# Performance work log

Hardware: AMD Instinct MI355X
Metric: run time of the kernel (lower is better)

## Reference

```python
import jax, jax.numpy as jnp
import numpy as np
from jax import lax

NB, D_MODEL, D_INNER, D_STATE, K, L, BATCH, NCLS, DT_RANK = 3, 512, 1024, 8, 4, 2048, 4, 10, 32


def setup_inputs() -> dict:
    key = jax.random.key(0)
    ks = jax.random.split(key, 12)
    s = 0.02
    inp = {
        "x": jax.random.normal(ks[0], (BATCH, L, D_MODEL), jnp.float32),
        "in_proj_w": s * jax.random.normal(ks[1], (NB, D_MODEL, 2 * D_INNER), jnp.float32),
        "conv_w": s * jax.random.normal(ks[2], (NB, D_INNER, K), jnp.float32),
        "conv_b": jnp.zeros((NB, D_INNER), jnp.float32),
        "x_proj_w": s * jax.random.normal(ks[3], (NB, D_INNER, DT_RANK + 2 * D_STATE), jnp.float32),
        "dt_proj_w": s * jax.random.normal(ks[4], (NB, DT_RANK, D_INNER), jnp.float32),
        "dt_proj_b": jnp.full((NB, D_INNER), -4.0, jnp.float32),
        "A_log": jnp.broadcast_to(jnp.log(jnp.arange(1, D_STATE + 1, dtype=jnp.float32)), (NB, D_INNER, D_STATE)).copy(),
        "D": jnp.ones((NB, D_INNER), jnp.float32),
        "out_proj_w": s * jax.random.normal(ks[5], (NB, D_INNER, D_MODEL), jnp.float32),
        "cls_w": s * jax.random.normal(ks[6], (D_MODEL, NCLS), jnp.float32),
        "cls_b": jnp.zeros((NCLS,), jnp.float32),
    }
    return inp


def _mamba_block(x, Wi, cw, cb, Wx, Wdt, bdt, A_log, Dp, Wo):
    # x: [B, L, d_model]
    Bsz, Lx, _ = x.shape
    d_inner = Dp.shape[0]
    d_state = A_log.shape[-1]
    dt_rank = Wdt.shape[0]
    xz = x @ Wi                               # [B, L, 2*d_inner]
    u, z = jnp.split(xz, 2, axis=-1)
    # causal depthwise conv1d over time
    uc = jnp.swapaxes(u, 1, 2)                # [B, d_inner, L]
    k = cw.shape[-1]
    uc = lax.conv_general_dilated(uc, cw[:, None, :], window_strides=(1,),
                                  padding=[(k - 1, 0)], feature_group_count=d_inner,
                                  dimension_numbers=("NCH", "OIH", "NCH"))
    u = jax.nn.silu(jnp.swapaxes(uc, 1, 2) + cb)   # [B, L, d_inner]
    dbl = u @ Wx                                   # [B, L, dt_rank + 2*d_state]
    dt = dbl[..., :dt_rank]
    Bm = dbl[..., dt_rank:dt_rank + d_state]
    Cm = dbl[..., dt_rank + d_state:]
    delta = jax.nn.softplus(dt @ Wdt + bdt)        # [B, L, d_inner]
    A = -jnp.exp(A_log)                            # [d_inner, d_state]

    def step(h, inp):
        d_t, B_t, C_t, u_t = inp                   # [B,d],[B,n],[B,n],[B,d]
        h = jnp.exp(d_t[..., None] * A) * h + (d_t * u_t)[..., None] * B_t[:, None, :]
        return h, jnp.einsum("bdn,bn->bd", h, C_t)

    xs = (jnp.swapaxes(delta, 0, 1), jnp.swapaxes(Bm, 0, 1),
          jnp.swapaxes(Cm, 0, 1), jnp.swapaxes(u, 0, 1))
    h0 = jnp.zeros((Bsz, d_inner, d_state), x.dtype)
    _, ys = lax.scan(step, h0, xs)                 # ys: [L, B, d_inner]
    y = jnp.swapaxes(ys, 0, 1) + u * Dp
    y = y * jax.nn.silu(z)
    return x + y @ Wo                              # residual


def reference(x, in_proj_w, conv_w, conv_b, x_proj_w, dt_proj_w, dt_proj_b, A_log, D, out_proj_w, cls_w, cls_b):
    nb = in_proj_w.shape[0]
    for i in range(nb):
        x = _mamba_block(x, in_proj_w[i], conv_w[i], conv_b[i], x_proj_w[i],
                         dt_proj_w[i], dt_proj_b[i], A_log[i], D[i], out_proj_w[i])
    pooled = jnp.mean(x, axis=1)                   # AdaptiveAvgPool1d(1) over seq
    return pooled @ cls_w + cls_b                  # [B, num_classes]
```

## Files before the change

### kernel.cpp

```cpp
#include <hip/hip_runtime.h>
#include <cstddef>
#include <cstdint>

#define L_SEQ   2048
#define BATCH_N 4
#define DMODEL  512
#define DINNER  1024
#define DSTATE  8
#define KCONV   4
#define DTRANK  32
#define NBLK    3
#define NCLS_N  10
#define MROWS   (BATCH_N * L_SEQ)
#define DBLW    48
#define NSPLIT  8

#define LC2 16
#define NC2 (L_SEQ / LC2)
#define DHALF (DINNER / 2)
#define SCAN_THREADS 512
#define SCAN_WAVES   (SCAN_THREADS / 64)

#define CGRP 8
#define CPG  (NC2 / CGRP)

typedef __attribute__((ext_vector_type(8))) short bf16x8;
typedef __attribute__((ext_vector_type(4))) short bf16x4;
typedef __attribute__((ext_vector_type(2))) short bf16x2;
typedef __attribute__((ext_vector_type(4))) float f32x4;

__device__ __forceinline__ float sigmoid_fast(float x) { return 1.f / (1.f + __expf(-x)); }
__device__ __forceinline__ float silu_fast(float x)    { return x * sigmoid_fast(x); }
__device__ __forceinline__ float softplus_fast(float x){
    return fmaxf(x, 0.f) + __logf(1.f + __expf(-fabsf(x)));
}
__device__ __forceinline__ float exp2_fast(float x) {
#if __has_builtin(__builtin_amdgcn_exp2f)
    return __builtin_amdgcn_exp2f(x);
#else
    return __expf(x * 0.69314718055994531f);
#endif
}
#define LOG2E 1.44269504088896341f

__device__ __forceinline__ unsigned short f2bf(float f) {
    union { float f; uint32_t u; } v; v.f = f;
    const uint32_t u = v.u;
    return (unsigned short)((u + 0x7fffu + ((u >> 16) & 1u)) >> 16);
}
__device__ __forceinline__ float bf2f(unsigned short h) {
    union { uint32_t u; float f; } v; v.u = ((uint32_t)h) << 16;
    return v.f;
}
__device__ __forceinline__ float bf2f_s(short h) { return bf2f((unsigned short)h); }

__device__ __forceinline__ void load_lds16(const void* g, void* l) {
    __builtin_amdgcn_global_load_lds(
        (const __attribute__((address_space(1))) unsigned int*)g,
        (__attribute__((address_space(3))) unsigned int*)l,
        16, 0, 0);
}

template <int K, int NT, int EPI>
__global__ __launch_bounds__(256) void gemm_bf16(
    const unsigned short* __restrict__ A, int lda,
    const unsigned short* __restrict__ Bt, int ldb,
    int ldc,
    unsigned short* __restrict__ Obf,
    float* __restrict__ pool)
{
    constexpr int BCH   = NT / 8;
    constexpr int NTW   = NT / 32;
    constexpr int STAGE = 8192 + NT * 64;
    constexpr int EPIL  = 128 * (NT + 8);
    constexpr int SMEM  = (STAGE > EPIL) ? STAGE : EPIL;
    __shared__ unsigned short sMem[SMEM];
    unsigned short* sA = sMem;
    unsigned short* sB = sMem + 8192;

    const int tid  = threadIdx.x;
    const int lane = tid & 63;
    const int wave = tid >> 6;

    const int nwgx = gridDim.x;
    const int nwg  = nwgx * gridDim.y;
    int flat = blockIdx.y * nwgx + blockIdx.x;
    {
        const int q = nwg >> 3, r = nwg & 7;
        const int xcd = flat & 7, lid = flat >> 3;
        flat = (xcd < r ? xcd * (q + 1) : r * (q + 1) + (xcd - r) * q) + lid;
    }
    const int m0 = (flat / nwgx) * 128;
    const int n0 = (flat % nwgx) * NT;

    const int wm = (wave >> 1) * 64;
    const int wn = (wave & 1) * (NT / 2);
    const int lm = lane & 15;
    const int lq = lane >> 4;

    const int srow = lane >> 3;
    const int scol = ((lane & 7) ^ srow) * 8;

    f32x4 acc[4][NTW];
    #pragma unroll
    for (int i = 0; i < 4; ++i)
        #pragma unroll
        for (int j = 0; j < NTW; ++j) acc[i][j] = (f32x4){0.f, 0.f, 0.f, 0.f};

    for (int k0 = 0; k0 < K; k0 += 64) {
        #pragma unroll
        for (int c = wave; c < 16; c += 4)
            load_lds16(A + (size_t)(m0 + c * 8 + srow) * lda + k0 + scol, &sA[c * 512]);
        #pragma unroll
        for (int c = wave; c < BCH; c += 4)
            load_lds16(Bt + (size_t)(n0 + c * 8 + srow) * ldb + k0 + scol, &sB[c * 512]);
        __syncthreads();
        #pragma unroll
        for (int ks = 0; ks < 2; ++ks) {
            bf16x8 aF[4], bF[NTW];
            #pragma unroll
            for (int mt = 0; mt < 4; ++mt) {
                const int row = wm + mt * 16 + lm;
                aF[mt] = *(const bf16x8*)&sA[row * 64 + (((ks * 4 + lq) ^ (lm & 7)) * 8)];
            }
            #pragma unroll
            for (int nt = 0; nt < NTW; ++nt) {
                const int row = wn + nt * 16 + lm;
                bF[nt] = *(const bf16x8*)&sB[row * 64 + (((ks * 4 + lq) ^ (lm & 7)) * 8)];
            }
            #pragma unroll
            for (int mt = 0; mt < 4; ++mt)
                #pragma unroll
                for (int nt = 0; nt < NTW; ++nt)
                    acc[mt][nt] = __builtin_amdgcn_mfma_f32_16x16x32_bf16(
                        aF[mt], bF[nt], acc[mt][nt], 0, 0, 0);
        }
        __syncthreads();
    }

    unsigned short* sOut = sMem;
    #pragma unroll
    for (int mt = 0; mt < 4; ++mt) {
        #pragma unroll
        for (int nt = 0; nt < NTW; ++nt) {
            #pragma unroll
            for (int r = 0; r < 4; ++r) {
                const int row = wm + mt * 16 + lq * 4 + r;
                const int col = wn + nt * 16 + lm;
                float v = acc[mt][nt][r];
                if (EPI >= 2) {
                    const size_t gi = (size_t)(m0 + row) * ldc + n0 + col;
                    v += bf2f(Obf[gi]);
                }
                sOut[row * (NT + 8) + col] = f2bf(v);
            }
        }
    }
    __syncthreads();
    #pragma unroll
    for (int j = 0; j < NT / 16; ++j) {
        const int idx = j * 256 + tid;
        const int row = idx / (NT / 8);
        const int cpos = (idx % (NT / 8)) * 8;
        *(bf16x8*)&Obf[(size_t)(m0 + row) * ldc + n0 + cpos] =
            *(const bf16x8*)&sOut[row * (NT + 8) + cpos];
    }
    if (EPI == 3) {
        const int b = m0 >> 11;
        const int col = tid & (NT - 1);
        const int q = tid / NT;
        constexpr int RPQ = 128 / (256 / NT);
        float s = 0.f;
        #pragma unroll
        for (int r = q * RPQ; r < (q + 1) * RPQ; ++r)
            s += bf2f(sOut[r * (NT + 8) + col]);
        atomicAdd(&pool[b * DMODEL + n0 + col], s);
    }
}

__global__ __launch_bounds__(256) void conv_xproj_kernel(
    const unsigned short* __restrict__ xz,
    const float* __restrict__ cwt,
    const float* __restrict__ cb,
    const unsigned short* __restrict__ Wxt,
    unsigned short* __restrict__ ub,
    float* __restrict__ Xp)
{
    __shared__ unsigned short sU[64 * 128];
    const int tid = threadIdx.x, lane = tid & 63, wave = tid >> 6;
    const int lm = lane & 15, lq = lane >> 4;
    const int row0 = blockIdx.x * 64;
    const int split = blockIdx.y;
    const int k0 = split * (DINNER / NSPLIT);

    const int cj  = tid & 15;
    const int rr0 = tid >> 4;
    const int dcol = k0 + cj * 8;
    float4 cb0 = *(const float4*)&cb[dcol];
    float4 cb1 = *(const float4*)&cb[dcol + 4];
    float4 w0[KCONV], w1[KCONV];
    #pragma unroll
    for (int k = 0; k < KCONV; ++k) {
        w0[k] = *(const float4*)&cwt[k * DINNER + dcol];
        w1[k] = *(const float4*)&cwt[k * DINNER + dcol + 4];
    }
    #pragma unroll
    for (int p = 0; p < 4; ++p) {
        const int rl = p * 16 + rr0;
        const int m  = row0 + rl;
        const int t  = m & (L_SEQ - 1);
        float acc[8];
        acc[0] = cb0.x; acc[1] = cb0.y; acc[2] = cb0.z; acc[3] = cb0.w;
        acc[4] = cb1.x; acc[5] = cb1.y; acc[6] = cb1.z; acc[7] = cb1.w;
        #pragma unroll
        for (int k = 0; k < KCONV; ++k) {
            if (t + k - (KCONV - 1) >= 0) {
                bf16x8 xv = *(const bf16x8*)&xz[(size_t)(m + k - (KCONV - 1)) * (2 * DINNER) + dcol];
                acc[0] = fmaf(bf2f_s(xv[0]), w0[k].x, acc[0]);
                acc[1] = fmaf(bf2f_s(xv[1]), w0[k].y, acc[1]);
                acc[2] = fmaf(bf2f_s(xv[2]), w0[k].z, acc[2]);
                acc[3] = fmaf(bf2f_s(xv[3]), w0[k].w, acc[3]);
                acc[4] = fmaf(bf2f_s(xv[4]), w1[k].x, acc[4]);
                acc[5] = fmaf(bf2f_s(xv[5]), w1[k].y, acc[5]);
                acc[6] = fmaf(bf2f_s(xv[6]), w1[k].z, acc[6]);
                acc[7] = fmaf(bf2f_s(xv[7]), w1[k].w, acc[7]);
            }
        }
        bf16x8 o;
        #pragma unroll
        for (int j = 0; j < 8; ++j) o[j] = (short)f2bf(silu_fast(acc[j]));
        *(bf16x8*)&ub[(size_t)m * DINNER + dcol] = o;
        *(bf16x8*)&sU[rl * 128 + ((cj ^ (rl & 7)) * 8)] = o;
    }
    __syncthreads();

    const int rowA = row0 + wave * 16;
    f32x4 acc3[3];
    #pragma unroll
    for (int j = 0; j < 3; ++j) acc3[j] = (f32x4){0.f, 0.f, 0.f, 0.f};

    #pragma unroll
    for (int kk = 0; kk < DINNER / NSPLIT; kk += 32) {
        const int rl = wave * 16 + lm;
        bf16x8 aF = *(const bf16x8*)&sU[rl * 128 + ((((kk >> 3) + lq) ^ (lm & 7)) * 8)];
        bf16x8 bF[3];
        #pragma unroll
        for (int nt = 0; nt < 3; ++nt)
            bF[nt] = *(const bf16x8*)&Wxt[(size_t)(nt * 16 + lm) * DINNER + k0 + kk + lq * 8];
        #pragma unroll
        for (int nt = 0; nt < 3; ++nt)
            acc3[nt] = __builtin_amdgcn_mfma_f32_16x16x32_bf16(
                aF, bF[nt], acc3[nt], 0, 0, 0);
    }
    float* dst = Xp + (size_t)split * MROWS * DBLW;
    #pragma unroll
    for (int nt = 0; nt < 3; ++nt)
        #pragma unroll
        for (int r = 0; r < 4; ++r)
            dst[(size_t)(rowA + lq * 4 + r) * DBLW + nt * 16 + lm] = acc3[nt][r];
}

__global__ __launch_bounds__(256) void xp_reduce(
    const float* __restrict__ Xp, float* __restrict__ dblsum)
{
    const int i = blockIdx.x * 256 + threadIdx.x;
    f32x4 s = (f32x4){0.f, 0.f, 0.f, 0.f};
    #pragma unroll
    for (int sp = 0; sp < NSPLIT; ++sp)
        s += ((const f32x4*)(Xp + (size_t)sp * MROWS * DBLW))[i];
    ((f32x4*)dblsum)[i] = s;
}

__global__ void prep_negA(const float* __restrict__ A_log, float* __restrict__ negA) {
    const int i = blockIdx.x * 256 + threadIdx.x;
    if (i < NBLK * DINNER * DSTATE)
        negA[i] = -__expf(A_log[i]) * LOG2E;
}

__global__ __launch_bounds__(256) void transpose_cast(
    const float* __restrict__ in, unsigned short* __restrict__ out,
    int Kdim, int Ndim, size_t in_stride, size_t out_stride)
{
    __shared__ float s[32][33];
    const float* ip = in + blockIdx.z * in_stride;
    unsigned short* op = out + blockIdx.z * out_stride;
    const int bx = blockIdx.x * 32;
    const int by = blockIdx.y * 32;
    const int t = threadIdx.x;
    const int r = t >> 3;
    const int c4 = (t & 7) * 4;

    const int row = by + r;
    if (bx + c4 + 3 < Ndim) {
        float4 v = *(const float4*)&ip[(size_t)row * Ndim + bx + c4];
        s[r][c4 + 0] = v.x; s[r][c4 + 1] = v.y; s[r][c4 + 2] = v.z; s[r][c4 + 3] = v.w;
    } else {
        for (int i = 0; i < 4; ++i) {
            const int col = bx + c4 + i;
            s[r][c4 + i] = (col < Ndim) ? ip[(size_t)row * Ndim + col] : 0.f;
        }
    }
    __syncthreads();
    if (bx + r < Ndim) {
        unsigned short w0 = f2bf(s[c4 + 0][r]), w1 = f2bf(s[c4 + 1][r]);
        unsigned short w2 = f2bf(s[c4 + 2][r]), w3 = f2bf(s[c4 + 3][r]);
        uint2 pk;
        pk.x = (uint32_t)w0 | ((uint32_t)w1 << 16);
        pk.y = (uint32_t)w2 | ((uint32_t)w3 << 16);
        *(uint2*)&op[(size_t)(bx + r) * Kdim + by + c4] = pk;
    }
}

__global__ void cast_init(const float* __restrict__ in, unsigned short* __restrict__ outb,
                          float* __restrict__ pooled_accum, int n4) {
    const int i = blockIdx.x * 256 + threadIdx.x;
    if (i < BATCH_N * DMODEL / 4)
        ((f32x4*)pooled_accum)[i] = (f32x4){0.f, 0.f, 0.f, 0.f};
    if (i >= n4) return;
    float4 v = ((const float4*)in)[i];
    uint2 pk;
    pk.x = (uint32_t)f2bf(v.x) | ((uint32_t)f2bf(v.y) << 16);
    pk.y = (uint32_t)f2bf(v.z) | ((uint32_t)f2bf(v.w) << 16);
    ((uint2*)outb)[i] = pk;
}

__global__ void conv_w_transpose(const float* __restrict__ cw, float* __restrict__ cwt) {
    const int i = blockIdx.x * 256 + threadIdx.x;
    if (i >= NBLK * DINNER * KCONV) return;
    const int blk = i >> 12;
    const int rem = i & 4095;
    const int d = rem >> 2;
    const int k = rem & 3;
    cwt[blk * 4096 + k * DINNER + d] = cw[blk * 4096 + d * KCONV + k];
}

__device__ __forceinline__ void dt_recompute_lds(
    unsigned short* sDelta,
    const float* __restrict__ dblsum,
    const unsigned short* __restrict__ Wdtt,
    const float* __restrict__ bdt,
    size_t m0, int lane, int wave, int dbase)
{
    const int lm = lane & 15, lq = lane >> 4;
    bf16x8 aF;
    {
        const float* p = &dblsum[(m0 + lm) * DBLW + lq * 8];
        float4 x0 = *(const float4*)p;
        float4 x1 = *(const float4*)(p + 4);
        aF[0] = (short)f2bf(x0.x); aF[1] = (short)f2bf(x0.y);
        aF[2] = (short)f2bf(x0.z); aF[3] = (short)f2bf(x0.w);
        aF[4] = (short)f2bf(x1.x); aF[5] = (short)f2bf(x1.y);
        aF[6] = (short)f2bf(x1.z); aF[7] = (short)f2bf(x1.w);
    }
    constexpr int NPW = DHALF / (16 * SCAN_WAVES);
    #pragma unroll
    for (int nt = 0; nt < NPW; ++nt) {
        const int cloc = wave * (DHALF / SCAN_WAVES) + nt * 16;
        const int col16 = dbase + cloc;
        bf16x8 bF = *(const bf16x8*)&Wdtt[(size_t)(col16 + lm) * DTRANK + lq * 8];
        f32x4 acc = (f32x4){0.f, 0.f, 0.f, 0.f};
        acc = __builtin_amdgcn_mfma_f32_16x16x32_bf16(aF, bF, acc, 0, 0, 0);
        const float bias = bdt[col16 + lm];
        #pragma unroll
        for (int r = 0; r < 4; ++r)
            sDelta[(lq * 4 + r) * DHALF + cloc + lm] =
                f2bf(softplus_fast(acc[r] + bias));
    }
}

__device__ __forceinline__ bool a_is_arange(const float* a) {
    bool pw = true;
    #pragma unroll
    for (int n = 1; n < DSTATE; ++n)
        pw = pw && (fabsf(a[n] - (float)(n + 1) * a[0]) <=
                    1e-5f * (float)(n + 1) * fabsf(a[0]));
    return pw;
}

__global__ __launch_bounds__(SCAN_THREADS) void scan_chunk_kernel(
    const unsigned short* __restrict__ ub,
    const float* __restrict__ dblsum,
    const unsigned short* __restrict__ Wdtt,
    const float* __restrict__ bdt,
    const float* __restrict__ negA,
    float* __restrict__ PSbuf)
{
    const int c  = blockIdx.x;
    const int dh = blockIdx.y;
    const int b  = blockIdx.z;
    const int tid = threadIdx.x;
    const int lane = tid & 63;
    const int wave = tid >> 6;
    const int dbase = dh * DHALF;
    const int d = dbase + tid;

    __shared__ unsigned short sDelta[LC2 * DHALF];
    __shared__ float sB[LC2][DSTATE];

    const size_t m0 = (size_t)b * L_SEQ + c * LC2;

    dt_recompute_lds(sDelta, dblsum, Wdtt, bdt, m0, lane, wave, dbase);
    if (tid < LC2 * DSTATE) {
        const int r = tid >> 3, n = tid & 7;
        sB[r][n] = dblsum[(m0 + r) * DBLW + DTRANK + n];
    }
    __syncthreads();

    float a[DSTATE], S[DSTATE];
    {
        float4 a0 = *(const float4*)&negA[(size_t)d * DSTATE];
        float4 a1 = *(const float4*)&negA[(size_t)d * DSTATE + 4];
        a[0] = a0.x; a[1] = a0.y; a[2] = a0.z; a[3] = a0.w;
        a[4] = a1.x; a[5] = a1.y; a[6] = a1.z; a[7] = a1.w;
    }
    #pragma unroll
    for (int n = 0; n < DSTATE; ++n) S[n] = 0.f;
    float dtsum = 0.f;

    if (a_is_arange(a)) {
        for (int r = 0; r < LC2; ++r) {
            const size_t m = m0 + r;
            const float dt = bf2f(sDelta[r * DHALF + tid]);
            const float du = dt * bf2f(ub[m * DINNER + d]);
            dtsum += dt;
            const float e1 = exp2_fast(dt * a[0]);
            float e = e1;
            #pragma unroll
            for (int n = 0; n < DSTATE; ++n) {
                S[n] = fmaf(e, S[n], du * sB[r][n]);
                e *= e1;
            }
        }
        const size_t nb = (size_t)(b * NC2 + c) * DSTATE;
        const float P1 = exp2_fast(a[0] * dtsum);
        float p = P1;
        #pragma unroll
        for (int n = 0; n < DSTATE; ++n) {
            float2 ps; ps.x = p; ps.y = S[n];
            *(float2*)&PSbuf[(nb + n) * (DINNER * 2) + (size_t)d * 2] = ps;
            p *= P1;
        }
    } else {
        for (int r = 0; r < LC2; ++r) {
            const size_t m = m0 + r;
            const float dt = bf2f(sDelta[r * DHALF + tid]);
            const float du = dt * bf2f(ub[m * DINNER + d]);
            dtsum += dt;
            #pragma unroll
            for (int n = 0; n < DSTATE; ++n) {
                const float e = exp2_fast(dt * a[n]);
                S[n] = fmaf(e, S[n], du * sB[r][n]);
            }
        }
        const size_t nb = (size_t)(b * NC2 + c) * DSTATE;
        #pragma unroll
        for (int n = 0; n < DSTATE; ++n) {
            float2 ps; ps.x = exp2_fast(a[n] * dtsum); ps.y = S[n];
            *(float2*)&PSbuf[(nb + n) * (DINNER * 2) + (size_t)d * 2] = ps;
        }
    }
}

__global__ __launch_bounds__(512) void scan_combine_kernel(
    const float* __restrict__ PSbuf,
    float* __restrict__ Hbuf)
{
    const int dl = threadIdx.x & 63;
    const int g  = threadIdx.x >> 6;
    const int d  = blockIdx.x * 64 + dl;
    const int n  = blockIdx.y;
    const int b  = blockIdx.z;

    __shared__ float sP[CGRP][64];
    __shared__ float sS[CGRP][64];

    const int c0 = g * CPG;
    float Pseg = 1.f, Sseg = 0.f;
    #pragma unroll 4
    for (int cc = 0; cc < CPG; ++cc) {
        const size_t row = (size_t)(b * NC2 + c0 + cc) * DSTATE + n;
        const float2 ps = *(const float2*)&PSbuf[row * (DINNER * 2) + (size_t)d * 2];
        Pseg *= ps.x;
        Sseg = fmaf(ps.x, Sseg, ps.y);
    }
    sP[g][dl] = Pseg;
    sS[g][dl] = Sseg;
    __syncthreads();

    float h = 0.f;
    for (int gg = 0; gg < g; ++gg)
        h = fmaf(sP[gg][dl], h, sS[gg][dl]);

    #pragma unroll 4
    for (int cc = 0; cc < CPG; ++cc) {
        const size_t row = (size_t)(b * NC2 + c0 + cc) * DSTATE + n;
        const float2 ps = *(const float2*)&PSbuf[row * (DINNER * 2) + (size_t)d * 2];
        Hbuf[row * DINNER + d] = h;
        h = fmaf(ps.x, h, ps.y);
    }
}

__global__ __launch_bounds__(SCAN_THREADS) void scan_out_kernel(
    const unsigned short* __restrict__ ub,
    const float* __restrict__ dblsum,
    const unsigned short* __restrict__ Wdtt,
    const float* __restrict__ bdt,
    const unsigned short* __restrict__ xz,
    const float* __restrict__ negA,
    const float* __restrict__ Dp,
    const float* __restrict__ Hin,
    unsigned short* __restrict__ ybuf)
{
    const int c  = blockIdx.x;
    const int dh = blockIdx.y;
    const int b  = blockIdx.z;
    const int tid = threadIdx.x;
    const int lane = tid & 63;
    const int wave = tid >> 6;
    const int dbase = dh * DHALF;
    const int d = dbase + tid;

    __shared__ unsigned short sDelta[LC2 * DHALF];
    __shared__ float sB[LC2][DSTATE];
    __shared__ float sC[LC2][DSTATE];

    const size_t m0 = (size_t)b * L_SEQ + c * LC2;

    dt_recompute_lds(sDelta, dblsum, Wdtt, bdt, m0, lane, wave, dbase);
    if (tid < LC2 * 2 * DSTATE) {
        const int r = tid >> 4, j = tid & 15;
        const float v = dblsum[(m0 + r) * DBLW + DTRANK + j];
        if (j < DSTATE) sB[r][j] = v;
        else            sC[r][j - DSTATE] = v;
    }
    __syncthreads();

    float a[DSTATE], h[DSTATE];
    {
        float4 a0 = *(const float4*)&negA[(size_t)d * DSTATE];
        float4 a1 = *(const float4*)&negA[(size_t)d * DSTATE + 4];
        a[0] = a0.x; a[1] = a0.y; a[2] = a0.z; a[3] = a0.w;
        a[4] = a1.x; a[5] = a1.y; a[6] = a1.z; a[7] = a1.w;
    }
    const size_t base = ((size_t)(b * NC2 + c) * DSTATE) * DINNER + d;
    #pragma unroll
    for (int n = 0; n < DSTATE; ++n)
        h[n] = Hin[base + (size_t)n * DINNER];
    const float Dd = Dp[d];

    if (a_is_arange(a)) {
        for (int r = 0; r < LC2; ++r) {
            const size_t m = m0 + r;
            const float dt = bf2f(sDelta[r * DHALF + tid]);
            const float ut = bf2f(ub[m * DINNER + d]);
            const float zt = bf2f(xz[m * (2 * DINNER) + DINNER + d]);
            const float du = dt * ut;
            const float e1 = exp2_fast(dt * a[0]);
            float e = e1;
            float acc = 0.f;
            #pragma unroll
            for (int n = 0; n < DSTATE; ++n) {
                h[n] = fmaf(e, h[n], du * sB[r][n]);
                acc = fmaf(h[n], sC[r][n], acc);
                e *= e1;
            }
            ybuf[m * DINNER + d] = f2bf(fmaf(ut, Dd, acc) * silu_fast(zt));
        }
    } else {
        for (int r = 0; r < LC2; ++r) {
            const size_t m = m0 + r;
            const float dt = bf2f(sDelta[r * DHALF + tid]);
            const float ut = bf2f(ub[m * DINNER + d]);
            const float zt = bf2f(xz[m * (2 * DINNER) + DINNER + d]);
            const float du = dt * ut;
            float acc = 0.f;
            #pragma unroll
            for (int n = 0; n < DSTATE; ++n) {
                const float e = exp2_fast(dt * a[n]);
                h[n] = fmaf(e, h[n], du * sB[r][n]);
                acc = fmaf(h[n], sC[r][n], acc);
            }
            ybuf[m * DINNER + d] = f2bf(fmaf(ut, Dd, acc) * silu_fast(zt));
        }
    }
}

__global__ __launch_bounds__(512) void pool_cls_kernel(
    const float* __restrict__ pooled_accum,
    const float* __restrict__ w,
    const float* __restrict__ bias,
    float* __restrict__ out)
{
    __shared__ float sp[DMODEL];
    const int b = blockIdx.x;
    const int dm = threadIdx.x;
    sp[dm] = pooled_accum[b * DMODEL + dm] * (1.f / (float)L_SEQ);
    __syncthreads();
    if (dm < NCLS_N) {
        float acc = bias[dm];
        for (int k = 0; k < DMODEL; ++k)
            acc = fmaf(sp[k], w[k * NCLS_N + dm], acc);
        out[b * NCLS_N + dm] = acc;
    }
}

extern "C" void kernel_launch(void* const* d_in, const int* in_sizes, int n_in,
                              void* d_out, int out_size, void* d_ws, size_t ws_size,
                              hipStream_t stream) {
    const float* x_in      = (const float*)d_in[0];
    const float* in_proj_w = (const float*)d_in[1];
    const float* conv_w    = (const float*)d_in[2];
    const float* conv_b    = (const float*)d_in[3];
    const float* x_proj_w  = (const float*)d_in[4];
    const float* dt_proj_w = (const float*)d_in[5];
    const float* dt_proj_b = (const float*)d_in[6];
    const float* A_log     = (const float*)d_in[7];
    const float* Dp        = (const float*)d_in[8];
    const float* out_proj_w= (const float*)d_in[9];
    const float* cls_w     = (const float*)d_in[10];
    const float* cls_b     = (const float*)d_in[11];
    float* out = (float*)d_out;

    char* w = (char*)d_ws;
    auto alloc = [&](size_t bytes) { char* p = w; w += (bytes + 255) & ~(size_t)255; return p; };
    unsigned short* xz_bf  = (unsigned short*)alloc((size_t)MROWS * 2 * DINNER * 2);
    unsigned short* ub     = (unsigned short*)alloc((size_t)MROWS * DINNER * 2);
    float*          Xp     = (float*)         alloc((size_t)NSPLIT * MROWS * DBLW * 4);
    float*          dblsum = (float*)         alloc((size_t)MROWS * DBLW * 4);
    float*          PSbuf  = (float*)         alloc((size_t)BATCH_N * NC2 * DSTATE * DINNER * 2 * 4);
    float*          Hbuf   = (float*)         alloc((size_t)BATCH_N * NC2 * DSTATE * DINNER * 4);
    unsigned short* xb     = (unsigned short*)alloc((size_t)MROWS * DMODEL * 2);
    unsigned short* ybuf   = (unsigned short*)alloc((size_t)MROWS * DINNER * 2);
    unsigned short* Wit    = (unsigned short*)alloc((size_t)NBLK * 2048 * 512 * 2);
    unsigned short* Wot    = (unsigned short*)alloc((size_t)NBLK * 512 * 1024 * 2);
    unsigned short* Wxt    = (unsigned short*)alloc((size_t)NBLK * DBLW * 1024 * 2);
    unsigned short* Wdtt   = (unsigned short*)alloc((size_t)NBLK * 1024 * DTRANK * 2);
    float*          cwt    = (float*)         alloc((size_t)NBLK * KCONV * DINNER * 4);
    float*          negA   = (float*)         alloc((size_t)NBLK * DINNER * DSTATE * 4);
    float*          pooled = (float*)         alloc((size_t)BATCH_N * DMODEL * 4);

    cast_init<<<(MROWS * DMODEL / 4) / 256, 256, 0, stream>>>(
        x_in, xb, pooled, MROWS * DMODEL / 4);
    transpose_cast<<<dim3(2048 / 32, 512 / 32, NBLK), 256, 0, stream>>>(
        in_proj_w, Wit, 512, 2048, (size_t)512 * 2048, (size_t)2048 * 512);
    transpose_cast<<<dim3(512 / 32, 1024 / 32, NBLK), 256, 0, stream>>>(
        out_proj_w, Wot, 1024, 512, (size_t)1024 * 512, (size_t)512 * 1024);
    transpose_cast<<<dim3(2, 1024 / 32, NBLK), 256, 0, stream>>>(
        x_proj_w, Wxt, 1024, DBLW, (size_t)1024 * DBLW, (size_t)DBLW * 1024);
    transpose_cast<<<dim3(1024 / 32, 1, NBLK), 256, 0, stream>>>(
        dt_proj_w, Wdtt, DTRANK, 1024, (size_t)DTRANK * 1024, (size_t)1024 * DTRANK);
    conv_w_transpose<<<(NBLK * DINNER * KCONV + 255) / 256, 256, 0, stream>>>(conv_w, cwt);
    prep_negA<<<(NBLK * DINNER * DSTATE + 255) / 256, 256, 0, stream>>>(A_log, negA);

    for (int blk = 0; blk < NBLK; ++blk) {
        const unsigned short* Wit_b  = Wit  + (size_t)blk * 2048 * 512;
        const unsigned short* Wot_b  = Wot  + (size_t)blk * 512 * 1024;
        const unsigned short* Wxt_b  = Wxt  + (size_t)blk * DBLW * 1024;
        const unsigned short* Wdtt_b = Wdtt + (size_t)blk * 1024 * DTRANK;
        const float* cwt_b = cwt + (size_t)blk * KCONV * DINNER;
        const float* cb  = conv_b    + (size_t)blk * DINNER;
        const float* bdt = dt_proj_b + (size_t)blk * DINNER;
        const float* nA  = negA      + (size_t)blk * DINNER * DSTATE;
        const float* Dv  = Dp        + (size_t)blk * DINNER;

        gemm_bf16<512, 128, 0><<<dim3(2048 / 128, MROWS / 128), 256, 0, stream>>>(
            xb, DMODEL, Wit_b, DMODEL, 2 * DINNER, xz_bf, nullptr);
        conv_xproj_kernel<<<dim3(MROWS / 64, NSPLIT), 256, 0, stream>>>(
            xz_bf, cwt_b, cb, Wxt_b, ub, Xp);
        xp_reduce<<<(MROWS * DBLW / 4) / 256, 256, 0, stream>>>(Xp, dblsum);
        {
            dim3 gridA(NC2, 2, BATCH_N);
            scan_chunk_kernel<<<gridA, SCAN_THREADS, 0, stream>>>(
                ub, dblsum, Wdtt_b, bdt, nA, PSbuf);
            scan_combine_kernel<<<dim3(DINNER / 64, DSTATE, BATCH_N), 512, 0, stream>>>(
                PSbuf, Hbuf);
            scan_out_kernel<<<gridA, SCAN_THREADS, 0, stream>>>(
                ub, dblsum, Wdtt_b, bdt, xz_bf, nA, Dv, Hbuf, ybuf);
        }
        if (blk < NBLK - 1)
            gemm_bf16<1024, 64, 2><<<dim3(DMODEL / 64, MROWS / 128), 256, 0, stream>>>(
                ybuf, DINNER, Wot_b, DINNER, DMODEL, xb, nullptr);
        else
            gemm_bf16<1024, 64, 3><<<dim3(DMODEL / 64, MROWS / 128), 256, 0, stream>>>(
                ybuf, DINNER, Wot_b, DINNER, DMODEL, xb, pooled);
    }

    pool_cls_kernel<<<BATCH_N, DMODEL, 0, stream>>>(pooled, cls_w, cls_b, out);
}
```

Baseline: 477.9 us.

## Fuse split-K reduction into scan kernels and merge prep kernels into cast_init

Removes the xp_reduce kernel. Each scan_chunk and scan_out block now sums the NSPLIT partial x_proj outputs for its own 16 rows straight into a padded LDS tile and reads dt, B and C from there. The one-time prep kernels for negA and the conv weight transpose are folded into cast_init, and scan_combine keeps its PS values in registers instead of reading them from global memory twice. In exchange, the split reduction is computed twice (once per scan kernel and once per d-half block), which adds redundant global reads of Xp. There is also an extra __syncthreads before the dt recompute.

```diff
diff --git a/kernel.cpp b/kernel.cpp
--- a/kernel.cpp
+++ b/kernel.cpp
@@ -20,6 +20,7 @@
 #define DHALF (DINNER / 2)
 #define SCAN_THREADS 512
 #define SCAN_WAVES   (SCAN_THREADS / 64)
+#define DBLP 52
 
 #define CGRP 8
 #define CPG  (NC2 / CGRP)
@@ -260,23 +261,6 @@
             dst[(size_t)(rowA + lq * 4 + r) * DBLW + nt * 16 + lm] = acc3[nt][r];
 }
 
-__global__ __launch_bounds__(256) void xp_reduce(
-    const float* __restrict__ Xp, float* __restrict__ dblsum)
-{
-    const int i = blockIdx.x * 256 + threadIdx.x;
-    f32x4 s = (f32x4){0.f, 0.f, 0.f, 0.f};
-    #pragma unroll
-    for (int sp = 0; sp < NSPLIT; ++sp)
-        s += ((const f32x4*)(Xp + (size_t)sp * MROWS * DBLW))[i];
-    ((f32x4*)dblsum)[i] = s;
-}
-
-__global__ void prep_negA(const float* __restrict__ A_log, float* __restrict__ negA) {
-    const int i = blockIdx.x * 256 + threadIdx.x;
-    if (i < NBLK * DINNER * DSTATE)
-        negA[i] = -__expf(A_log[i]) * LOG2E;
-}
-
 __global__ __launch_bounds__(256) void transpose_cast(
     const float* __restrict__ in, unsigned short* __restrict__ out,
     int Kdim, int Ndim, size_t in_stride, size_t out_stride)
@@ -312,10 +296,22 @@
 }
 
 __global__ void cast_init(const float* __restrict__ in, unsigned short* __restrict__ outb,
-                          float* __restrict__ pooled_accum, int n4) {
+                          float* __restrict__ pooled_accum,
+                          const float* __restrict__ A_log, float* __restrict__ negA,
+                          const float* __restrict__ cw, float* __restrict__ cwt,
+                          int n4) {
     const int i = blockIdx.x * 256 + threadIdx.x;
     if (i < BATCH_N * DMODEL / 4)
         ((f32x4*)pooled_accum)[i] = (f32x4){0.f, 0.f, 0.f, 0.f};
+    if (i < NBLK * DINNER * DSTATE)
+        negA[i] = -__expf(A_log[i]) * LOG2E;
+    if (i < NBLK * DINNER * KCONV) {
+        const int blk = i >> 12;
+        const int rem = i & 4095;
+        const int d = rem >> 2;
+        const int k = rem & 3;
+        cwt[blk * 4096 + k * DINNER + d] = cw[blk * 4096 + d * KCONV + k];
+    }
     if (i >= n4) return;
     float4 v = ((const float4*)in)[i];
     uint2 pk;
@@ -324,27 +320,17 @@
     ((uint2*)outb)[i] = pk;
 }
 
-__global__ void conv_w_transpose(const float* __restrict__ cw, float* __restrict__ cwt) {
-    const int i = blockIdx.x * 256 + threadIdx.x;
-    if (i >= NBLK * DINNER * KCONV) return;
-    const int blk = i >> 12;
-    const int rem = i & 4095;
-    const int d = rem >> 2;
-    const int k = rem & 3;
-    cwt[blk * 4096 + k * DINNER + d] = cw[blk * 4096 + d * KCONV + k];
-}
-
 __device__ __forceinline__ void dt_recompute_lds(
     unsigned short* sDelta,
-    const float* __restrict__ dblsum,
+    const float* sDbl,
     const unsigned short* __restrict__ Wdtt,
     const float* __restrict__ bdt,
-    size_t m0, int lane, int wave, int dbase)
+    int lane, int wave, int dbase)
 {
     const int lm = lane & 15, lq = lane >> 4;
     bf16x8 aF;
     {
-        const float* p = &dblsum[(m0 + lm) * DBLW + lq * 8];
+        const float* p = &sDbl[lm * DBLP + lq * 8];
         float4 x0 = *(const float4*)p;
         float4 x1 = *(const float4*)(p + 4);
         aF[0] = (short)f2bf(x0.x); aF[1] = (short)f2bf(x0.y);
@@ -368,6 +354,19 @@
     }
 }
 
+__device__ __forceinline__ void stage_dbl_rows(
+    float* sDbl, const float* __restrict__ Xp, size_t m0, int tid)
+{
+    for (int idx = tid; idx < LC2 * DBLW; idx += SCAN_THREADS) {
+        const int mr = idx / DBLW, j = idx - mr * DBLW;
+        float s = 0.f;
+        #pragma unroll
+        for (int sp = 0; sp < NSPLIT; ++sp)
+            s += Xp[((size_t)sp * MROWS + m0 + mr) * DBLW + j];
+        sDbl[mr * DBLP + j] = s;
+    }
+}
+
 __device__ __forceinline__ bool a_is_arange(const float* a) {
     bool pw = true;
     #pragma unroll
@@ -379,7 +378,7 @@
 
 __global__ __launch_bounds__(SCAN_THREADS) void scan_chunk_kernel(
     const unsigned short* __restrict__ ub,
-    const float* __restrict__ dblsum,
+    const float* __restrict__ Xp,
     const unsigned short* __restrict__ Wdtt,
     const float* __restrict__ bdt,
     const float* __restrict__ negA,
@@ -395,15 +394,13 @@
     const int d = dbase + tid;
 
     __shared__ unsigned short sDelta[LC2 * DHALF];
-    __shared__ float sB[LC2][DSTATE];
+    __shared__ float sDbl[LC2 * DBLP];
 
     const size_t m0 = (size_t)b * L_SEQ + c * LC2;
 
-    dt_recompute_lds(sDelta, dblsum, Wdtt, bdt, m0, lane, wave, dbase);
-    if (tid < LC2 * DSTATE) {
-        const int r = tid >> 3, n = tid & 7;
-        sB[r][n] = dblsum[(m0 + r) * DBLW + DTRANK + n];
-    }
+    stage_dbl_rows(sDbl, Xp, m0, tid);
+    __syncthreads();
+    dt_recompute_lds(sDelta, sDbl, Wdtt, bdt, lane, wave, dbase);
     __syncthreads();
 
     float a[DSTATE], S[DSTATE];
@@ -427,7 +424,7 @@
             float e = e1;
             #pragma unroll
             for (int n = 0; n < DSTATE; ++n) {
-                S[n] = fmaf(e, S[n], du * sB[r][n]);
+                S[n] = fmaf(e, S[n], du * sDbl[r * DBLP + DTRANK + n]);
                 e *= e1;
             }
         }
@@ -449,7 +446,7 @@
             #pragma unroll
             for (int n = 0; n < DSTATE; ++n) {
                 const float e = exp2_fast(dt * a[n]);
-                S[n] = fmaf(e, S[n], du * sB[r][n]);
+                S[n] = fmaf(e, S[n], du * sDbl[r * DBLP + DTRANK + n]);
             }
         }
         const size_t nb = (size_t)(b * NC2 + c) * DSTATE;
@@ -475,13 +472,14 @@
     __shared__ float sS[CGRP][64];
 
     const int c0 = g * CPG;
+    float2 psr[CPG];
     float Pseg = 1.f, Sseg = 0.f;
-    #pragma unroll 4
+    #pragma unroll
     for (int cc = 0; cc < CPG; ++cc) {
         const size_t row = (size_t)(b * NC2 + c0 + cc) * DSTATE + n;
-        const float2 ps = *(const float2*)&PSbuf[row * (DINNER * 2) + (size_t)d * 2];
-        Pseg *= ps.x;
-        Sseg = fmaf(ps.x, Sseg, ps.y);
+        psr[cc] = *(const float2*)&PSbuf[row * (DINNER * 2) + (size_t)d * 2];
+        Pseg *= psr[cc].x;
+        Sseg = fmaf(psr[cc].x, Sseg, psr[cc].y);
     }
     sP[g][dl] = Pseg;
     sS[g][dl] = Sseg;
@@ -491,18 +489,17 @@
     for (int gg = 0; gg < g; ++gg)
         h = fmaf(sP[gg][dl], h, sS[gg][dl]);
 
-    #pragma unroll 4
+    #pragma unroll
     for (int cc = 0; cc < CPG; ++cc) {
         const size_t row = (size_t)(b * NC2 + c0 + cc) * DSTATE + n;
-        const float2 ps = *(const float2*)&PSbuf[row * (DINNER * 2) + (size_t)d * 2];
         Hbuf[row * DINNER + d] = h;
-        h = fmaf(ps.x, h, ps.y);
+        h = fmaf(psr[cc].x, h, psr[cc].y);
     }
 }
 
 __global__ __launch_bounds__(SCAN_THREADS) void scan_out_kernel(
     const unsigned short* __restrict__ ub,
-    const float* __restrict__ dblsum,
+    const float* __restrict__ Xp,
     const unsigned short* __restrict__ Wdtt,
     const float* __restrict__ bdt,
     const unsigned short* __restrict__ xz,
@@ -521,18 +518,13 @@
     const int d = dbase + tid;
 
     __shared__ unsigned short sDelta[LC2 * DHALF];
-    __shared__ float sB[LC2][DSTATE];
-    __shared__ float sC[LC2][DSTATE];
+    __shared__ float sDbl[LC2 * DBLP];
 
     const size_t m0 = (size_t)b * L_SEQ + c * LC2;
 
-    dt_recompute_lds(sDelta, dblsum, Wdtt, bdt, m0, lane, wave, dbase);
-    if (tid < LC2 * 2 * DSTATE) {
-        const int r = tid >> 4, j = tid & 15;
-        const float v = dblsum[(m0 + r) * DBLW + DTRANK + j];
-        if (j < DSTATE) sB[r][j] = v;
-        else            sC[r][j - DSTATE] = v;
-    }
+    stage_dbl_rows(sDbl, Xp, m0, tid);
+    __syncthreads();
+    dt_recompute_lds(sDelta, sDbl, Wdtt, bdt, lane, wave, dbase);
     __syncthreads();
 
     float a[DSTATE], h[DSTATE];
@@ -560,8 +552,8 @@
             float acc = 0.f;
             #pragma unroll
             for (int n = 0; n < DSTATE; ++n) {
-                h[n] = fmaf(e, h[n], du * sB[r][n]);
-                acc = fmaf(h[n], sC[r][n], acc);
+                h[n] = fmaf(e, h[n], du * sDbl[r * DBLP + DTRANK + n]);
+                acc = fmaf(h[n], sDbl[r * DBLP + DTRANK + DSTATE + n], acc);
                 e *= e1;
             }
             ybuf[m * DINNER + d] = f2bf(fmaf(ut, Dd, acc) * silu_fast(zt));
@@ -577,8 +569,8 @@
             #pragma unroll
             for (int n = 0; n < DSTATE; ++n) {
                 const float e = exp2_fast(dt * a[n]);
-                h[n] = fmaf(e, h[n], du * sB[r][n]);
-                acc = fmaf(h[n], sC[r][n], acc);
+                h[n] = fmaf(e, h[n], du * sDbl[r * DBLP + DTRANK + n]);
+                acc = fmaf(h[n], sDbl[r * DBLP + DTRANK + DSTATE + n], acc);
             }
             ybuf[m * DINNER + d] = f2bf(fmaf(ut, Dd, acc) * silu_fast(zt));
         }
@@ -626,7 +618,6 @@
     unsigned short* xz_bf  = (unsigned short*)alloc((size_t)MROWS * 2 * DINNER * 2);
     unsigned short* ub     = (unsigned short*)alloc((size_t)MROWS * DINNER * 2);
     float*          Xp     = (float*)         alloc((size_t)NSPLIT * MROWS * DBLW * 4);
-    float*          dblsum = (float*)         alloc((size_t)MROWS * DBLW * 4);
     float*          PSbuf  = (float*)         alloc((size_t)BATCH_N * NC2 * DSTATE * DINNER * 2 * 4);
     float*          Hbuf   = (float*)         alloc((size_t)BATCH_N * NC2 * DSTATE * DINNER * 4);
     unsigned short* xb     = (unsigned short*)alloc((size_t)MROWS * DMODEL * 2);
@@ -640,7 +631,7 @@
     float*          pooled = (float*)         alloc((size_t)BATCH_N * DMODEL * 4);
 
     cast_init<<<(MROWS * DMODEL / 4) / 256, 256, 0, stream>>>(
-        x_in, xb, pooled, MROWS * DMODEL / 4);
+        x_in, xb, pooled, A_log, negA, conv_w, cwt, MROWS * DMODEL / 4);
     transpose_cast<<<dim3(2048 / 32, 512 / 32, NBLK), 256, 0, stream>>>(
         in_proj_w, Wit, 512, 2048, (size_t)512 * 2048, (size_t)2048 * 512);
     transpose_cast<<<dim3(512 / 32, 1024 / 32, NBLK), 256, 0, stream>>>(
@@ -649,8 +640,6 @@
         x_proj_w, Wxt, 1024, DBLW, (size_t)1024 * DBLW, (size_t)DBLW * 1024);
     transpose_cast<<<dim3(1024 / 32, 1, NBLK), 256, 0, stream>>>(
         dt_proj_w, Wdtt, DTRANK, 1024, (size_t)DTRANK * 1024, (size_t)1024 * DTRANK);
-    conv_w_transpose<<<(NBLK * DINNER * KCONV + 255) / 256, 256, 0, stream>>>(conv_w, cwt);
-    prep_negA<<<(NBLK * DINNER * DSTATE + 255) / 256, 256, 0, stream>>>(A_log, negA);
 
     for (int blk = 0; blk < NBLK; ++blk) {
         const unsigned short* Wit_b  = Wit  + (size_t)blk * 2048 * 512;
@@ -667,15 +656,14 @@
             xb, DMODEL, Wit_b, DMODEL, 2 * DINNER, xz_bf, nullptr);
         conv_xproj_kernel<<<dim3(MROWS / 64, NSPLIT), 256, 0, stream>>>(
             xz_bf, cwt_b, cb, Wxt_b, ub, Xp);
-        xp_reduce<<<(MROWS * DBLW / 4) / 256, 256, 0, stream>>>(Xp, dblsum);
         {
             dim3 gridA(NC2, 2, BATCH_N);
             scan_chunk_kernel<<<gridA, SCAN_THREADS, 0, stream>>>(
-                ub, dblsum, Wdtt_b, bdt, nA, PSbuf);
+                ub, Xp, Wdtt_b, bdt, nA, PSbuf);
             scan_combine_kernel<<<dim3(DINNER / 64, DSTATE, BATCH_N), 512, 0, stream>>>(
                 PSbuf, Hbuf);
             scan_out_kernel<<<gridA, SCAN_THREADS, 0, stream>>>(
-                ub, dblsum, Wdtt_b, bdt, xz_bf, nA, Dv, Hbuf, ybuf);
+                ub, Xp, Wdtt_b, bdt, xz_bf, nA, Dv, Hbuf, ybuf);
         }
         if (blk < NBLK - 1)
             gemm_bf16<1024, 64, 2><<<dim3(DMODEL / 64, MROWS / 128), 256, 0, stream>>>(
```

Result: faster. 463.7 us (-3.0%).
